# Optimization experiments

Measured on AMD Instinct MI355X. Metric: run time of the kernel, lower is better.

## Reference

```python
import jax, jax.numpy as jnp
import numpy as np

N, E, F, D, G = 50000, 800000, 64, 64, 512
BN_EPS = 1e-5


def setup_inputs() -> dict:
    key = jax.random.key(0)
    ks = jax.random.split(key, 12)
    inp = {
        "x": jax.random.normal(ks[0], (N, F), dtype=jnp.float32),
        "edge_index": jax.random.randint(ks[1], (2, E), 0, N, dtype=jnp.int32),
        "batch": jnp.sort(jax.random.randint(ks[2], (N,), 0, G, dtype=jnp.int32)),
    }
    s = 0.05
    inp.update({
        "w1_a": jax.random.normal(ks[3], (F, D), jnp.float32) * s, "b1_a": jnp.zeros((D,), jnp.float32),
        "w1_b": jax.random.normal(ks[4], (D, D), jnp.float32) * s, "b1_b": jnp.zeros((D,), jnp.float32),
        "g1": jnp.ones((D,), jnp.float32), "be1": jnp.zeros((D,), jnp.float32),
        "w2_a": jax.random.normal(ks[5], (D, D), jnp.float32) * s, "b2_a": jnp.zeros((D,), jnp.float32),
        "w2_b": jax.random.normal(ks[6], (D, D), jnp.float32) * s, "b2_b": jnp.zeros((D,), jnp.float32),
        "g2": jnp.ones((D,), jnp.float32), "be2": jnp.zeros((D,), jnp.float32),
        "w3_a": jax.random.normal(ks[7], (D, D), jnp.float32) * s, "b3_a": jnp.zeros((D,), jnp.float32),
        "w3_b": jax.random.normal(ks[8], (D, D), jnp.float32) * s, "b3_b": jnp.zeros((D,), jnp.float32),
        "g3": jnp.ones((D,), jnp.float32), "be3": jnp.zeros((D,), jnp.float32),
        "w_lin0": jax.random.normal(ks[9], (D, 2 * D), jnp.float32) * s, "b_lin0": jnp.zeros((2 * D,), jnp.float32),
        "w_fc1": jax.random.normal(ks[10], (2 * D, D), jnp.float32) * s, "b_fc1": jnp.zeros((D,), jnp.float32),
    })
    return inp


def _gin_bn_layer(h, edge_index, w_a, b_a, w_b, b_b, gamma, beta):
    # GINConv (eps=0): nn(x + sum_{j->i} x_j); message = x[src] scattered to dst
    agg = jax.ops.segment_sum(h[edge_index[0]], edge_index[1], num_segments=h.shape[0])
    z = agg + h
    z = jnp.maximum(z @ w_a + b_a, 0.0) @ w_b + b_b  # inner MLP
    z = jnp.maximum(z, 0.0)                           # F.relu after conv
    mean = jnp.mean(z, axis=0)                        # BatchNorm1d, training stats
    var = jnp.mean((z - mean) ** 2, axis=0)
    return (z - mean) * jax.lax.rsqrt(var + BN_EPS) * gamma + beta


def reference(x, edge_index, batch,
              w1_a, b1_a, w1_b, b1_b, g1, be1,
              w2_a, b2_a, w2_b, b2_b, g2, be2,
              w3_a, b3_a, w3_b, b3_b, g3, be3,
              w_lin0, b_lin0, w_fc1, b_fc1):
    h = _gin_bn_layer(x, edge_index, w1_a, b1_a, w1_b, b1_b, g1, be1)
    h = _gin_bn_layer(h, edge_index, w2_a, b2_a, w2_b, b2_b, g2, be2)
    h = _gin_bn_layer(h, edge_index, w3_a, b3_a, w3_b, b3_b, g3, be3)
    xpool = jax.ops.segment_sum(h, batch, num_segments=G)  # global_add_pool [G, D]
    out = xpool @ w_lin0 + b_lin0                           # GINEncoder.lin0 -> [G, 2D]
    out = jnp.maximum(out @ w_fc1 + b_fc1, 0.0)             # relu(fc1); fc2 output is discarded (show_embedding=True)
    return out
```

## Files before the change

kernel.cpp:

```cpp
#include <hip/hip_runtime.h>

#define NN 50000
#define EE 800000
#define DD 64
#define GG 512
#define TILES 782
#define SCAN_BLOCKS 98
#define TS 68

__device__ __forceinline__ float b2f(unsigned short u) {
    union { unsigned int i; float f; } c;
    c.i = ((unsigned int)u) << 16;
    return c.f;
}
__device__ __forceinline__ unsigned short f2b(float f) {
    union { float f; unsigned int i; } c;
    c.f = f;
    const unsigned int r = c.i + 0x7FFFu + ((c.i >> 16) & 1u);
    return (unsigned short)(r >> 16);
}
__device__ __forceinline__ int rfl(int v) { return __builtin_amdgcn_readfirstlane(v); }

__global__ __launch_bounds__(256) void hist_kernel(const int* __restrict__ ei,
                                                   int* __restrict__ counts) {
    const int e = blockIdx.x * blockDim.x + threadIdx.x;
    if (e < EE) atomicAdd(&counts[ei[EE + e]], 1);
}

__global__ __launch_bounds__(512) void scan1_kernel(const int* __restrict__ counts,
                                                    int* __restrict__ scanned,
                                                    int* __restrict__ bsum) {
    __shared__ int buf[512];
    const int i = blockIdx.x * 512 + threadIdx.x;
    const int v = (i < NN) ? counts[i] : 0;
    buf[threadIdx.x] = v;
    __syncthreads();
    for (int off = 1; off < 512; off <<= 1) {
        const int add = (threadIdx.x >= off) ? buf[threadIdx.x - off] : 0;
        __syncthreads();
        buf[threadIdx.x] += add;
        __syncthreads();
    }
    if (i < NN) scanned[i] = buf[threadIdx.x] - v;
    if (threadIdx.x == 511) bsum[blockIdx.x] = buf[511];
}

__global__ __launch_bounds__(512) void scan2_kernel(const int* __restrict__ scanned,
                                                    const int* __restrict__ bsum,
                                                    int* __restrict__ rowptr,
                                                    int* __restrict__ cursor) {
    __shared__ int red[128];
    if (threadIdx.x < 128)
        red[threadIdx.x] = (threadIdx.x < blockIdx.x) ? bsum[threadIdx.x] : 0;
    __syncthreads();
    for (int off = 64; off > 0; off >>= 1) {
        if (threadIdx.x < off) red[threadIdx.x] += red[threadIdx.x + off];
        __syncthreads();
    }
    const int offset = red[0];
    const int i = blockIdx.x * 512 + threadIdx.x;
    if (i < NN) {
        const int p = scanned[i] + offset;
        rowptr[i] = p;
        cursor[i] = p;
    }
    if (blockIdx.x == 0 && threadIdx.x == 0) rowptr[NN] = EE;
}

__global__ __launch_bounds__(256) void fill_kernel(const int* __restrict__ ei,
                                                   int* __restrict__ cursor,
                                                   int* __restrict__ col) {
    const int cls = blockIdx.x & 7;
    const int chunk = blockIdx.x >> 3;
    const int e0 = chunk * 3125;
    for (int e = e0 + threadIdx.x; e < e0 + 3125; e += 256) {
        const int dst = ei[EE + e];
        if (dst / 6250 == cls) {
            const int pos = atomicAdd(&cursor[dst], 1);
            col[pos] = ei[e];
        }
    }
}

__global__ __launch_bounds__(256) void tobf_kernel(const float* __restrict__ in,
                                                   unsigned short* __restrict__ out,
                                                   const int n4) {
    const int i = blockIdx.x * 256 + threadIdx.x;
    if (i >= n4) return;
    const float4 v = ((const float4*)in)[i];
    ushort4 o;
    o.x = f2b(v.x); o.y = f2b(v.y); o.z = f2b(v.z); o.w = f2b(v.w);
    ((ushort4*)out)[i] = o;
}

__global__ __launch_bounds__(256, 4) void gather_kernel(const unsigned short* __restrict__ hin,
                                                        const int* __restrict__ rowptr,
                                                        const int* __restrict__ col,
                                                        const float* __restrict__ ss,
                                                        const int apply,
                                                        float* __restrict__ z) {
    const int wv = (blockIdx.x * 256 + threadIdx.x) >> 6;
    const int lane = threadIdx.x & 63;
    const int row = rfl(wv);
    if (row >= NN) return;
    const float scl = apply ? ss[lane] : 1.0f;
    const float sft = apply ? ss[64 + lane] : 0.0f;

    const int beg = rfl(rowptr[row]);
    const int end = rfl(rowptr[row + 1]);
    const int deg = end - beg;
    float a[8];
    #pragma unroll
    for (int i = 0; i < 8; ++i) a[i] = 0.f;
    a[0] = b2f(hin[row * 64 + lane]);

    if (deg <= 16) {
        const int safeb = (beg < EE) ? beg : 0;
        int c[16];
        #pragma unroll
        for (int i = 0; i < 16; ++i) {
            const int jj = (i < deg) ? (beg + i) : safeb;
            c[i] = rfl(col[jj]);
        }
        float hv[16];
        #pragma unroll
        for (int i = 0; i < 16; ++i) hv[i] = b2f(hin[c[i] * 64 + lane]);
        #pragma unroll
        for (int i = 0; i < 16; ++i) a[i & 7] += (i < deg) ? hv[i] : 0.f;
    } else if (deg <= 32) {
        const int safeb = beg;
        int c[32];
        #pragma unroll
        for (int i = 0; i < 32; ++i) {
            const int jj = (i < deg) ? (beg + i) : safeb;
            c[i] = rfl(col[jj]);
        }
        float hv[32];
        #pragma unroll
        for (int i = 0; i < 32; ++i) hv[i] = b2f(hin[c[i] * 64 + lane]);
        #pragma unroll
        for (int i = 0; i < 32; ++i) a[i & 7] += (i < deg) ? hv[i] : 0.f;
    } else {
        int j = beg;
        for (; j + 16 <= end; j += 16) {
            int c[16];
            #pragma unroll
            for (int i = 0; i < 16; ++i) c[i] = rfl(col[j + i]);
            float hv[16];
            #pragma unroll
            for (int i = 0; i < 16; ++i) hv[i] = b2f(hin[c[i] * 64 + lane]);
            #pragma unroll
            for (int i = 0; i < 16; ++i) a[i & 7] += hv[i];
        }
        if (j < end) {
            int c[16];
            #pragma unroll
            for (int i = 0; i < 16; ++i) {
                const int jj = (j + i < end) ? (j + i) : beg;
                c[i] = rfl(col[jj]);
            }
            float hv[16];
            #pragma unroll
            for (int i = 0; i < 16; ++i) hv[i] = b2f(hin[c[i] * 64 + lane]);
            #pragma unroll
            for (int i = 0; i < 16; ++i) a[i & 7] += (j + i < end) ? hv[i] : 0.f;
        }
    }
    const float sum = ((a[0] + a[1]) + (a[2] + a[3])) + ((a[4] + a[5]) + (a[6] + a[7]));
    z[row * 64 + lane] = fmaf(sum, scl, (float)(deg + 1) * sft);
}

__global__ __launch_bounds__(512) void mlp_kernel(const float* __restrict__ z,
                                                  const float* __restrict__ wa,
                                                  const float* __restrict__ ba,
                                                  const float* __restrict__ wb,
                                                  const float* __restrict__ bb,
                                                  unsigned short* __restrict__ tout,
                                                  float* __restrict__ stats) {
    __shared__ float tile[64 * TS];
    __shared__ float tile2[64 * TS];
    __shared__ float red[8][128];

    const int wave = threadIdx.x >> 6;
    const int lane = threadIdx.x & 63;
    const int row0 = blockIdx.x * 64;
    const int nrows = min(64, NN - row0);

    #pragma unroll
    for (int m = 0; m < 2; ++m) {
        const int g = m * 512 + threadIdx.x;
        const int r = g >> 4;
        const int f = (g & 15) * 4;
        const int grow = row0 + r;
        float4 v = make_float4(0.f, 0.f, 0.f, 0.f);
        if (grow < NN) v = *(const float4*)(z + grow * 64 + f);
        *(float4*)(&tile[r * TS + f]) = v;
    }
    __syncthreads();

    const int f0 = rfl(wave * 8);
    float acc[8];
    #pragma unroll
    for (int j = 0; j < 8; ++j) acc[j] = ba[f0 + j];
    #pragma unroll 4
    for (int k4 = 0; k4 < 16; ++k4) {
        const float4 v = *(const float4*)(&tile[lane * TS + k4 * 4]);
        #pragma unroll
        for (int j = 0; j < 8; ++j) {
            acc[j] = fmaf(v.x, wa[(k4 * 4 + 0) * 64 + f0 + j], acc[j]);
            acc[j] = fmaf(v.y, wa[(k4 * 4 + 1) * 64 + f0 + j], acc[j]);
            acc[j] = fmaf(v.z, wa[(k4 * 4 + 2) * 64 + f0 + j], acc[j]);
            acc[j] = fmaf(v.w, wa[(k4 * 4 + 3) * 64 + f0 + j], acc[j]);
        }
    }
    #pragma unroll
    for (int j = 0; j < 8; j += 4) {
        float4 o;
        o.x = fmaxf(acc[j + 0], 0.f);
        o.y = fmaxf(acc[j + 1], 0.f);
        o.z = fmaxf(acc[j + 2], 0.f);
        o.w = fmaxf(acc[j + 3], 0.f);
        *(float4*)(&tile2[lane * TS + f0 + j]) = o;
    }
    __syncthreads();

    #pragma unroll
    for (int j = 0; j < 8; ++j) acc[j] = bb[f0 + j];
    #pragma unroll 4
    for (int k4 = 0; k4 < 16; ++k4) {
        const float4 v = *(const float4*)(&tile2[lane * TS + k4 * 4]);
        #pragma unroll
        for (int j = 0; j < 8; ++j) {
            acc[j] = fmaf(v.x, wb[(k4 * 4 + 0) * 64 + f0 + j], acc[j]);
            acc[j] = fmaf(v.y, wb[(k4 * 4 + 1) * 64 + f0 + j], acc[j]);
            acc[j] = fmaf(v.z, wb[(k4 * 4 + 2) * 64 + f0 + j], acc[j]);
            acc[j] = fmaf(v.w, wb[(k4 * 4 + 3) * 64 + f0 + j], acc[j]);
        }
    }
    #pragma unroll
    for (int j = 0; j < 8; j += 4) {
        float4 o;
        o.x = fmaxf(acc[j + 0], 0.f);
        o.y = fmaxf(acc[j + 1], 0.f);
        o.z = fmaxf(acc[j + 2], 0.f);
        o.w = fmaxf(acc[j + 3], 0.f);
        *(float4*)(&tile[lane * TS + f0 + j]) = o;
    }
    __syncthreads();

    {
        const int rbeg = wave * 8;
        const int rend = min(rbeg + 8, nrows);
        float s = 0.f, sq = 0.f;
        for (int r = rbeg; r < rend; ++r) {
            const float v = tile[r * TS + lane];
            s += v;
            sq += v * v;
        }
        red[wave][lane] = s;
        red[wave][64 + lane] = sq;
    }
    __syncthreads();
    if (threadIdx.x < 128) {
        float tot = 0.f;
        #pragma unroll
        for (int w = 0; w < 8; ++w) tot += red[w][threadIdx.x];
        atomicAdd(&stats[(blockIdx.x & 7) * 128 + threadIdx.x], tot);
    }

    #pragma unroll
    for (int m = 0; m < 2; ++m) {
        const int g = m * 512 + threadIdx.x;
        const int r = g >> 4;
        const int f = (g & 15) * 4;
        const int grow = row0 + r;
        if (grow < NN) {
            const float4 v = *(const float4*)(&tile[r * TS + f]);
            ushort4 o;
            o.x = f2b(v.x); o.y = f2b(v.y); o.z = f2b(v.z); o.w = f2b(v.w);
            *(ushort4*)(tout + grow * 64 + f) = o;
        }
    }
}

__global__ __launch_bounds__(128) void finalize_kernel(const float* __restrict__ stats,
                                                       const float* __restrict__ g,
                                                       const float* __restrict__ be,
                                                       float* __restrict__ ss) {
    __shared__ float red[128];
    const int f = threadIdx.x;
    float tot = 0.f;
    #pragma unroll
    for (int k = 0; k < 8; ++k) tot += stats[k * 128 + f];
    red[f] = tot;
    __syncthreads();
    if (f < 64) {
        const float mean = red[f] * (1.0f / NN);
        const float var = red[64 + f] * (1.0f / NN) - mean * mean;
        const float scl = g[f] * rsqrtf(var + 1e-5f);
        ss[f] = scl;
        ss[64 + f] = be[f] - mean * scl;
    }
}

__global__ __launch_bounds__(256) void pool_kernel(const unsigned short* __restrict__ t,
                                                   const int* __restrict__ batch,
                                                   const float* __restrict__ ss,
                                                   float* __restrict__ xpool) {
    const int wv = (blockIdx.x * 256 + threadIdx.x) >> 6;
    const int lane = threadIdx.x & 63;
    const int r0 = wv * 64;
    if (r0 >= NN) return;
    const int r1 = min(r0 + 64, NN);
    const float scl = ss[lane];
    const float sft = ss[64 + lane];
    int gprev = batch[r0];
    float acc = 0.f;
    for (int r = r0; r < r1; ++r) {
        const int g = batch[r];
        if (g != gprev) {
            __hip_atomic_fetch_add(&xpool[gprev * 64 + lane], acc,
                                   __ATOMIC_RELAXED, __HIP_MEMORY_SCOPE_AGENT);
            acc = 0.f;
            gprev = g;
        }
        acc += fmaf(b2f(t[r * 64 + lane]), scl, sft);
    }
    __hip_atomic_fetch_add(&xpool[gprev * 64 + lane], acc,
                           __ATOMIC_RELAXED, __HIP_MEMORY_SCOPE_AGENT);
}

__global__ __launch_bounds__(128) void head_kernel(const float* __restrict__ xpool,
                                                   const float* __restrict__ w0,
                                                   const float* __restrict__ b0,
                                                   const float* __restrict__ w1,
                                                   const float* __restrict__ b1,
                                                   float* __restrict__ out) {
    __shared__ float xp[64];
    __shared__ float midl[128];
    const int g = blockIdx.x;
    const int t = threadIdx.x;
    if (t < 64) xp[t] = xpool[g * 64 + t];
    __syncthreads();
    float acc = b0[t];
    #pragma unroll 8
    for (int k = 0; k < 64; ++k) acc = fmaf(xp[k], w0[k * 128 + t], acc);
    midl[t] = acc;
    __syncthreads();
    if (t < 64) {
        float a2 = b1[t];
        #pragma unroll 8
        for (int k = 0; k < 128; ++k) a2 = fmaf(midl[k], w1[k * 64 + t], a2);
        out[g * 64 + t] = fmaxf(a2, 0.f);
    }
}

extern "C" void kernel_launch(void* const* d_in, const int* in_sizes, int n_in,
                              void* d_out, int out_size, void* d_ws, size_t ws_size,
                              hipStream_t stream) {
    const float* x = (const float*)d_in[0];
    const int* ei = (const int*)d_in[1];
    const int* batch = (const int*)d_in[2];

    int* ibase   = (int*)d_ws;
    int* counts  = ibase;
    int* scanned = ibase + 50000;
    int* rowptr  = ibase + 100000;
    int* cursor  = ibase + 150004;
    int* bsum    = ibase + 200004;
    int* col     = ibase + 200132;
    float* fbase = (float*)d_ws + 1000192;
    float* stats = fbase;
    float* xpool = stats + 3072;
    float* ss    = xpool + 32768;
    float* z     = ss + 128;
    unsigned short* xbf  = (unsigned short*)(z + 3200000);
    unsigned short* t0bf = xbf + 3200000;
    unsigned short* t1bf = t0bf + 3200000;

    hipMemsetAsync(counts, 0, 50000 * sizeof(int), stream);
    hipMemsetAsync(stats, 0, (3072 + 32768) * sizeof(float), stream);
    hist_kernel<<<(EE + 255) / 256, 256, 0, stream>>>(ei, counts);
    scan1_kernel<<<SCAN_BLOCKS, 512, 0, stream>>>(counts, scanned, bsum);
    scan2_kernel<<<SCAN_BLOCKS, 512, 0, stream>>>(scanned, bsum, rowptr, cursor);
    fill_kernel<<<2048, 256, 0, stream>>>(ei, cursor, col);
    tobf_kernel<<<(800000 + 255) / 256, 256, 0, stream>>>(x, xbf, 800000);

    const unsigned short* hcur = xbf;
    unsigned short* touts[3] = {t0bf, t1bf, t0bf};
    for (int l = 0; l < 3; ++l) {
        const float* wa = (const float*)d_in[3 + l * 6 + 0];
        const float* ba = (const float*)d_in[3 + l * 6 + 1];
        const float* wb = (const float*)d_in[3 + l * 6 + 2];
        const float* bb = (const float*)d_in[3 + l * 6 + 3];
        const float* ga = (const float*)d_in[3 + l * 6 + 4];
        const float* be = (const float*)d_in[3 + l * 6 + 5];

        gather_kernel<<<12500, 256, 0, stream>>>(hcur, rowptr, col, ss, l > 0, z);
        mlp_kernel<<<TILES, 512, 0, stream>>>(z, wa, ba, wb, bb, touts[l],
                                              stats + l * 1024);
        finalize_kernel<<<1, 128, 0, stream>>>(stats + l * 1024, ga, be, ss);
        hcur = touts[l];
    }

    pool_kernel<<<(TILES + 3) / 4, 256, 0, stream>>>(t0bf, batch, ss, xpool);
    head_kernel<<<GG, 128, 0, stream>>>(
        xpool, (const float*)d_in[21], (const float*)d_in[22],
        (const float*)d_in[23], (const float*)d_in[24], (float*)d_out);
}
```

Baseline: 363.5 us.

## Use bf16 MFMA for GIN MLP, fuse BN finalize, merge prep kernels

Replaces the scalar-FMA fp32 two-layer MLP with bf16 MFMA 16x16x32 instructions, using weights pre-swizzled into fragment layout by a new wprep kernel. The gather output z is now stored as bf16, halving its traffic. The BatchNorm finalize kernel is folded into the MLP kernel through a last-block-done atomic counter, and the memsets plus the x-to-bf16 conversion are merged into one prep kernel. This trades fp32 accuracy in the MLP inputs for tensor-core throughput and fewer launches, and relies on a global completion counter with a fence to order the stats reduction.

```diff
diff --git a/kernel.cpp b/kernel.cpp
--- a/kernel.cpp
+++ b/kernel.cpp
@@ -6,7 +6,9 @@
 #define GG 512
 #define TILES 782
 #define SCAN_BLOCKS 98
-#define TS 68
+
+typedef __attribute__((ext_vector_type(8))) short short8;
+typedef __attribute__((ext_vector_type(4))) float f32x4;
 
 __device__ __forceinline__ float b2f(unsigned short u) {
     union { unsigned int i; float f; } c;
@@ -20,6 +22,46 @@
     return (unsigned short)(r >> 16);
 }
 __device__ __forceinline__ int rfl(int v) { return __builtin_amdgcn_readfirstlane(v); }
+
+__global__ __launch_bounds__(256) void prep_kernel(const float* __restrict__ x,
+                                                   unsigned short* __restrict__ xbf,
+                                                   int* __restrict__ counts,
+                                                   float* __restrict__ zblock) {
+    const int tid = blockIdx.x * 256 + threadIdx.x;
+    if (tid < 800000) {
+        const float4 v = ((const float4*)x)[tid];
+        ushort4 o;
+        o.x = f2b(v.x); o.y = f2b(v.y); o.z = f2b(v.z); o.w = f2b(v.w);
+        ((ushort4*)xbf)[tid] = o;
+    } else if (tid < 812500) {
+        ((int4*)counts)[tid - 800000] = make_int4(0, 0, 0, 0);
+    } else if (tid < 821464) {
+        ((float4*)zblock)[tid - 812500] = make_float4(0.f, 0.f, 0.f, 0.f);
+    }
+}
+
+__global__ __launch_bounds__(256) void wprep_kernel(const float* __restrict__ w0,
+                                                    const float* __restrict__ w1,
+                                                    const float* __restrict__ w2,
+                                                    const float* __restrict__ w3,
+                                                    const float* __restrict__ w4,
+                                                    const float* __restrict__ w5,
+                                                    unsigned short* __restrict__ out) {
+    const float* ws[6] = {w0, w1, w2, w3, w4, w5};
+    const float* w = ws[blockIdx.x];
+    unsigned short* o = out + blockIdx.x * 4096;
+    #pragma unroll
+    for (int it = 0; it < 2; ++it) {
+        const int idx = it * 256 + threadIdx.x;
+        const int fid = idx >> 6, lane = idx & 63;
+        const int kt = fid >> 2, nt = fid & 3;
+        const int kbase = kt * 32 + (lane >> 4) * 8;
+        const int n = nt * 16 + (lane & 15);
+        #pragma unroll
+        for (int j = 0; j < 8; ++j)
+            o[idx * 8 + j] = f2b(w[(kbase + j) * 64 + n]);
+    }
+}
 
 __global__ __launch_bounds__(256) void hist_kernel(const int* __restrict__ ei,
                                                    int* __restrict__ counts) {
@@ -82,23 +124,12 @@
     }
 }
 
-__global__ __launch_bounds__(256) void tobf_kernel(const float* __restrict__ in,
-                                                   unsigned short* __restrict__ out,
-                                                   const int n4) {
-    const int i = blockIdx.x * 256 + threadIdx.x;
-    if (i >= n4) return;
-    const float4 v = ((const float4*)in)[i];
-    ushort4 o;
-    o.x = f2b(v.x); o.y = f2b(v.y); o.z = f2b(v.z); o.w = f2b(v.w);
-    ((ushort4*)out)[i] = o;
-}
-
 __global__ __launch_bounds__(256, 4) void gather_kernel(const unsigned short* __restrict__ hin,
                                                         const int* __restrict__ rowptr,
                                                         const int* __restrict__ col,
                                                         const float* __restrict__ ss,
                                                         const int apply,
-                                                        float* __restrict__ z) {
+                                                        unsigned short* __restrict__ z) {
     const int wv = (blockIdx.x * 256 + threadIdx.x) >> 6;
     const int lane = threadIdx.x & 63;
     const int row = rfl(wv);
@@ -128,11 +159,10 @@
         #pragma unroll
         for (int i = 0; i < 16; ++i) a[i & 7] += (i < deg) ? hv[i] : 0.f;
     } else if (deg <= 32) {
-        const int safeb = beg;
         int c[32];
         #pragma unroll
         for (int i = 0; i < 32; ++i) {
-            const int jj = (i < deg) ? (beg + i) : safeb;
+            const int jj = (i < deg) ? (beg + i) : beg;
             c[i] = rfl(col[jj]);
         }
         float hv[32];
@@ -167,139 +197,133 @@
         }
     }
     const float sum = ((a[0] + a[1]) + (a[2] + a[3])) + ((a[4] + a[5]) + (a[6] + a[7]));
-    z[row * 64 + lane] = fmaf(sum, scl, (float)(deg + 1) * sft);
-}
-
-__global__ __launch_bounds__(512) void mlp_kernel(const float* __restrict__ z,
-                                                  const float* __restrict__ wa,
+    z[row * 64 + lane] = f2b(fmaf(sum, scl, (float)(deg + 1) * sft));
+}
+
+__global__ __launch_bounds__(256) void mlp_kernel(const unsigned short* __restrict__ z,
+                                                  const unsigned short* __restrict__ wfa,
                                                   const float* __restrict__ ba,
-                                                  const float* __restrict__ wb,
+                                                  const unsigned short* __restrict__ wfb,
                                                   const float* __restrict__ bb,
                                                   unsigned short* __restrict__ tout,
-                                                  float* __restrict__ stats) {
-    __shared__ float tile[64 * TS];
-    __shared__ float tile2[64 * TS];
-    __shared__ float red[8][128];
+                                                  float* __restrict__ stats,
+                                                  const float* __restrict__ ga,
+                                                  const float* __restrict__ be,
+                                                  float* __restrict__ ss,
+                                                  int* __restrict__ done) {
+    __shared__ unsigned short ldsT[4][16][72];
+    __shared__ float red[512];
+    __shared__ int lastflag;
 
     const int wave = threadIdx.x >> 6;
     const int lane = threadIdx.x & 63;
-    const int row0 = blockIdx.x * 64;
-    const int nrows = min(64, NN - row0);
-
-    #pragma unroll
-    for (int m = 0; m < 2; ++m) {
-        const int g = m * 512 + threadIdx.x;
+    const int quad = lane >> 4;
+    const int l15 = lane & 15;
+    const int rowbase = blockIdx.x * 64 + wave * 16;
+    const bool valid = rowbase < NN;
+
+    short8 wA[8], wB[8];
+    #pragma unroll
+    for (int f = 0; f < 8; ++f) {
+        wA[f] = *(const short8*)(wfa + (f * 64 + lane) * 8);
+        wB[f] = *(const short8*)(wfb + (f * 64 + lane) * 8);
+    }
+    float biasA[4], biasB[4];
+    #pragma unroll
+    for (int nt = 0; nt < 4; ++nt) {
+        biasA[nt] = ba[nt * 16 + l15];
+        biasB[nt] = bb[nt * 16 + l15];
+    }
+
+    const int arow = valid ? (rowbase + l15) : 0;
+    const short8 a0 = *(const short8*)(z + arow * 64 + quad * 8);
+    const short8 a1 = *(const short8*)(z + arow * 64 + 32 + quad * 8);
+
+    f32x4 acc[4];
+    #pragma unroll
+    for (int nt = 0; nt < 4; ++nt) {
+        f32x4 c = {0.f, 0.f, 0.f, 0.f};
+        c = __builtin_amdgcn_mfma_f32_16x16x32_bf16(a0, wA[nt], c, 0, 0, 0);
+        c = __builtin_amdgcn_mfma_f32_16x16x32_bf16(a1, wA[4 + nt], c, 0, 0, 0);
+        acc[nt] = c;
+    }
+    #pragma unroll
+    for (int nt = 0; nt < 4; ++nt)
+        #pragma unroll
+        for (int r = 0; r < 4; ++r)
+            ldsT[wave][quad * 4 + r][nt * 16 + l15] =
+                f2b(fmaxf(acc[nt][r] + biasA[nt], 0.f));
+
+    const short8 y0 = *(const short8*)(&ldsT[wave][l15][quad * 8]);
+    const short8 y1 = *(const short8*)(&ldsT[wave][l15][32 + quad * 8]);
+
+    #pragma unroll
+    for (int nt = 0; nt < 4; ++nt) {
+        f32x4 c = {0.f, 0.f, 0.f, 0.f};
+        c = __builtin_amdgcn_mfma_f32_16x16x32_bf16(y0, wB[nt], c, 0, 0, 0);
+        c = __builtin_amdgcn_mfma_f32_16x16x32_bf16(y1, wB[4 + nt], c, 0, 0, 0);
+        acc[nt] = c;
+    }
+    #pragma unroll
+    for (int nt = 0; nt < 4; ++nt)
+        #pragma unroll
+        for (int r = 0; r < 4; ++r)
+            ldsT[wave][quad * 4 + r][nt * 16 + l15] =
+                f2b(fmaxf(acc[nt][r] + biasB[nt], 0.f));
+
+    {
+        float s = 0.f, sq = 0.f;
+        if (valid) {
+            #pragma unroll 4
+            for (int r = 0; r < 16; ++r) {
+                const float v = b2f(ldsT[wave][r][lane]);
+                s += v;
+                sq += v * v;
+            }
+        }
+        red[wave * 128 + lane] = s;
+        red[wave * 128 + 64 + lane] = sq;
+    }
+    __syncthreads();
+
+    if (threadIdx.x < 128) {
+        const float tot = red[threadIdx.x] + red[128 + threadIdx.x] +
+                          red[256 + threadIdx.x] + red[384 + threadIdx.x];
+        atomicAdd(&stats[(blockIdx.x & 7) * 128 + threadIdx.x], tot);
+    }
+
+    #pragma unroll
+    for (int m = 0; m < 4; ++m) {
+        const int g = m * 256 + threadIdx.x;
         const int r = g >> 4;
-        const int f = (g & 15) * 4;
-        const int grow = row0 + r;
-        float4 v = make_float4(0.f, 0.f, 0.f, 0.f);
-        if (grow < NN) v = *(const float4*)(z + grow * 64 + f);
-        *(float4*)(&tile[r * TS + f]) = v;
-    }
-    __syncthreads();
-
-    const int f0 = rfl(wave * 8);
-    float acc[8];
-    #pragma unroll
-    for (int j = 0; j < 8; ++j) acc[j] = ba[f0 + j];
-    #pragma unroll 4
-    for (int k4 = 0; k4 < 16; ++k4) {
-        const float4 v = *(const float4*)(&tile[lane * TS + k4 * 4]);
-        #pragma unroll
-        for (int j = 0; j < 8; ++j) {
-            acc[j] = fmaf(v.x, wa[(k4 * 4 + 0) * 64 + f0 + j], acc[j]);
-            acc[j] = fmaf(v.y, wa[(k4 * 4 + 1) * 64 + f0 + j], acc[j]);
-            acc[j] = fmaf(v.z, wa[(k4 * 4 + 2) * 64 + f0 + j], acc[j]);
-            acc[j] = fmaf(v.w, wa[(k4 * 4 + 3) * 64 + f0 + j], acc[j]);
-        }
-    }
-    #pragma unroll
-    for (int j = 0; j < 8; j += 4) {
-        float4 o;
-        o.x = fmaxf(acc[j + 0], 0.f);
-        o.y = fmaxf(acc[j + 1], 0.f);
-        o.z = fmaxf(acc[j + 2], 0.f);
-        o.w = fmaxf(acc[j + 3], 0.f);
-        *(float4*)(&tile2[lane * TS + f0 + j]) = o;
-    }
-    __syncthreads();
-
-    #pragma unroll
-    for (int j = 0; j < 8; ++j) acc[j] = bb[f0 + j];
-    #pragma unroll 4
-    for (int k4 = 0; k4 < 16; ++k4) {
-        const float4 v = *(const float4*)(&tile2[lane * TS + k4 * 4]);
-        #pragma unroll
-        for (int j = 0; j < 8; ++j) {
-            acc[j] = fmaf(v.x, wb[(k4 * 4 + 0) * 64 + f0 + j], acc[j]);
-            acc[j] = fmaf(v.y, wb[(k4 * 4 + 1) * 64 + f0 + j], acc[j]);
-            acc[j] = fmaf(v.z, wb[(k4 * 4 + 2) * 64 + f0 + j], acc[j]);
-            acc[j] = fmaf(v.w, wb[(k4 * 4 + 3) * 64 + f0 + j], acc[j]);
-        }
-    }
-    #pragma unroll
-    for (int j = 0; j < 8; j += 4) {
-        float4 o;
-        o.x = fmaxf(acc[j + 0], 0.f);
-        o.y = fmaxf(acc[j + 1], 0.f);
-        o.z = fmaxf(acc[j + 2], 0.f);
-        o.w = fmaxf(acc[j + 3], 0.f);
-        *(float4*)(&tile[lane * TS + f0 + j]) = o;
-    }
-    __syncthreads();
-
-    {
-        const int rbeg = wave * 8;
-        const int rend = min(rbeg + 8, nrows);
-        float s = 0.f, sq = 0.f;
-        for (int r = rbeg; r < rend; ++r) {
-            const float v = tile[r * TS + lane];
-            s += v;
-            sq += v * v;
-        }
-        red[wave][lane] = s;
-        red[wave][64 + lane] = sq;
-    }
-    __syncthreads();
-    if (threadIdx.x < 128) {
+        const int f4 = (g & 15) * 4;
+        const int grow = blockIdx.x * 64 + r;
+        if (grow < NN)
+            *(ushort4*)(tout + grow * 64 + f4) =
+                *(const ushort4*)(&ldsT[r >> 4][r & 15][f4]);
+    }
+
+    __threadfence();
+    if (threadIdx.x == 0)
+        lastflag = (atomicAdd(done, 1) == (int)gridDim.x - 1) ? 1 : 0;
+    __syncthreads();
+    if (lastflag) {
         float tot = 0.f;
-        #pragma unroll
-        for (int w = 0; w < 8; ++w) tot += red[w][threadIdx.x];
-        atomicAdd(&stats[(blockIdx.x & 7) * 128 + threadIdx.x], tot);
-    }
-
-    #pragma unroll
-    for (int m = 0; m < 2; ++m) {
-        const int g = m * 512 + threadIdx.x;
-        const int r = g >> 4;
-        const int f = (g & 15) * 4;
-        const int grow = row0 + r;
-        if (grow < NN) {
-            const float4 v = *(const float4*)(&tile[r * TS + f]);
-            ushort4 o;
-            o.x = f2b(v.x); o.y = f2b(v.y); o.z = f2b(v.z); o.w = f2b(v.w);
-            *(ushort4*)(tout + grow * 64 + f) = o;
-        }
-    }
-}
-
-__global__ __launch_bounds__(128) void finalize_kernel(const float* __restrict__ stats,
-                                                       const float* __restrict__ g,
-                                                       const float* __restrict__ be,
-                                                       float* __restrict__ ss) {
-    __shared__ float red[128];
-    const int f = threadIdx.x;
-    float tot = 0.f;
-    #pragma unroll
-    for (int k = 0; k < 8; ++k) tot += stats[k * 128 + f];
-    red[f] = tot;
-    __syncthreads();
-    if (f < 64) {
-        const float mean = red[f] * (1.0f / NN);
-        const float var = red[64 + f] * (1.0f / NN) - mean * mean;
-        const float scl = g[f] * rsqrtf(var + 1e-5f);
-        ss[f] = scl;
-        ss[64 + f] = be[f] - mean * scl;
+        if (threadIdx.x < 128) {
+            #pragma unroll
+            for (int k = 0; k < 8; ++k)
+                tot += __hip_atomic_load(&stats[k * 128 + threadIdx.x],
+                                         __ATOMIC_RELAXED, __HIP_MEMORY_SCOPE_AGENT);
+            red[threadIdx.x] = tot;
+        }
+        __syncthreads();
+        if (threadIdx.x < 64) {
+            const float mean = red[threadIdx.x] * (1.0f / NN);
+            const float var = red[64 + threadIdx.x] * (1.0f / NN) - mean * mean;
+            const float scl = ga[threadIdx.x] * rsqrtf(var + 1e-5f);
+            ss[threadIdx.x] = scl;
+            ss[64 + threadIdx.x] = be[threadIdx.x] - mean * scl;
+        }
     }
 }
 
@@ -372,34 +396,38 @@
     float* fbase = (float*)d_ws + 1000192;
     float* stats = fbase;
     float* xpool = stats + 3072;
-    float* ss    = xpool + 32768;
-    float* z     = ss + 128;
-    unsigned short* xbf  = (unsigned short*)(z + 3200000);
+    int*   done  = (int*)(xpool + 32768);
+    float* ss    = xpool + 32768 + 16;
+    unsigned short* zbf  = (unsigned short*)(fbase + 35856 + 128);
+    unsigned short* xbf  = zbf + 3200000;
     unsigned short* t0bf = xbf + 3200000;
     unsigned short* t1bf = t0bf + 3200000;
-
-    hipMemsetAsync(counts, 0, 50000 * sizeof(int), stream);
-    hipMemsetAsync(stats, 0, (3072 + 32768) * sizeof(float), stream);
+    unsigned short* wfrag = t1bf + 3200000;
+
+    prep_kernel<<<(821464 + 255) / 256, 256, 0, stream>>>(x, xbf, counts, stats);
+    wprep_kernel<<<6, 256, 0, stream>>>(
+        (const float*)d_in[3], (const float*)d_in[5],
+        (const float*)d_in[9], (const float*)d_in[11],
+        (const float*)d_in[15], (const float*)d_in[17], wfrag);
     hist_kernel<<<(EE + 255) / 256, 256, 0, stream>>>(ei, counts);
     scan1_kernel<<<SCAN_BLOCKS, 512, 0, stream>>>(counts, scanned, bsum);
     scan2_kernel<<<SCAN_BLOCKS, 512, 0, stream>>>(scanned, bsum, rowptr, cursor);
     fill_kernel<<<2048, 256, 0, stream>>>(ei, cursor, col);
-    tobf_kernel<<<(800000 + 255) / 256, 256, 0, stream>>>(x, xbf, 800000);
 
     const unsigned short* hcur = xbf;
     unsigned short* touts[3] = {t0bf, t1bf, t0bf};
     for (int l = 0; l < 3; ++l) {
-        const float* wa = (const float*)d_in[3 + l * 6 + 0];
         const float* ba = (const float*)d_in[3 + l * 6 + 1];
-        const float* wb = (const float*)d_in[3 + l * 6 + 2];
         const float* bb = (const float*)d_in[3 + l * 6 + 3];
         const float* ga = (const float*)d_in[3 + l * 6 + 4];
         const float* be = (const float*)d_in[3 + l * 6 + 5];
 
-        gather_kernel<<<12500, 256, 0, stream>>>(hcur, rowptr, col, ss, l > 0, z);
-        mlp_kernel<<<TILES, 512, 0, stream>>>(z, wa, ba, wb, bb, touts[l],
-                                              stats + l * 1024);
-        finalize_kernel<<<1, 128, 0, stream>>>(stats + l * 1024, ga, be, ss);
+        gather_kernel<<<12500, 256, 0, stream>>>(hcur, rowptr, col, ss, l > 0, zbf);
+        mlp_kernel<<<TILES, 256, 0, stream>>>(zbf,
+                                              wfrag + (l * 2 + 0) * 4096, ba,
+                                              wfrag + (l * 2 + 1) * 4096, bb,
+                                              touts[l], stats + l * 1024,
+                                              ga, be, ss, done + l);
         hcur = touts[l];
     }
 
```

New measurement: 521.5 us. 1.43x slower.
